# Performance work log

Measured on AMD Instinct MI355X. Metric: run time of the kernel, lower is better.

## Reference

```python
import jax, jax.numpy as jnp
import numpy as np

N = 100000
E = 1600000
D_IN = 128
D_OUT = 128
HEADS = 4
C = D_OUT // HEADS  # per-head channels = 32
NEG_SLOPE = 0.2
EPS_SOFTMAX = 1e-16
EPS_LN = 1e-5


def setup_inputs() -> dict:
    key = jax.random.key(0)
    ks = jax.random.split(key, 10)
    x = jax.random.normal(ks[0], (N, D_IN), dtype=jnp.float32)
    edge_index = jax.random.randint(ks[1], (2, E), 0, N, dtype=jnp.int64)
    s = 1.0 / np.sqrt(D_IN)
    W = jax.random.normal(ks[2], (D_IN, HEADS * C), dtype=jnp.float32) * s
    att_src = jax.random.normal(ks[3], (HEADS, C), dtype=jnp.float32) * (1.0 / np.sqrt(C))
    att_dst = jax.random.normal(ks[4], (HEADS, C), dtype=jnp.float32) * (1.0 / np.sqrt(C))
    gat_bias = jax.random.normal(ks[5], (D_OUT,), dtype=jnp.float32) * 0.02
    skip_W = jax.random.normal(ks[6], (D_IN, D_OUT), dtype=jnp.float32) * s
    skip_b = jax.random.normal(ks[7], (D_OUT,), dtype=jnp.float32) * 0.02
    ln_g = jnp.ones((D_OUT,), dtype=jnp.float32)
    ln_b = jnp.zeros((D_OUT,), dtype=jnp.float32)
    return {"x": x, "edge_index": edge_index, "W": W, "att_src": att_src,
            "att_dst": att_dst, "gat_bias": gat_bias, "skip_W": skip_W,
            "skip_b": skip_b, "ln_g": ln_g, "ln_b": ln_b}


def _gat_edge_conv(x, src, dst, W, att_src, att_dst, gat_bias, skip_W, skip_b, ln_g, ln_b):
    n = x.shape[0]
    h = (x @ W).reshape(n, HEADS, C)                      # [N,H,C]
    a_s = jnp.einsum('nhc,hc->nh', h, att_src)            # [N,H]
    a_d = jnp.einsum('nhc,hc->nh', h, att_dst)            # [N,H]
    e = jax.nn.leaky_relu(a_s[src] + a_d[dst], NEG_SLOPE)  # [E,H]
    # segment softmax over incoming edges of each dst node
    m = jax.ops.segment_max(e, dst, num_segments=n)        # [N,H]
    p = jnp.exp(e - m[dst])
    z = jax.ops.segment_sum(p, dst, num_segments=n)        # [N,H]
    alpha = p / (z[dst] + EPS_SOFTMAX)                     # [E,H]
    msg = h[src] * alpha[:, :, None]                       # [E,H,C]
    out = jax.ops.segment_sum(msg, dst, num_segments=n)    # [N,H,C]
    out = out.reshape(n, HEADS * C) + gat_bias
    out = out + x @ skip_W + skip_b
    mu = out.mean(-1, keepdims=True)
    var = ((out - mu) ** 2).mean(-1, keepdims=True)
    return (out - mu) * jax.lax.rsqrt(var + EPS_LN) * ln_g + ln_b


def reference(x, edge_index, W, att_src, att_dst, gat_bias, skip_W, skip_b, ln_g, ln_b):
    n = x.shape[0]
    loops = jnp.arange(n, dtype=edge_index.dtype)          # PyG GATConv add_self_loops=True
    src = jnp.concatenate([edge_index[0], loops])
    dst = jnp.concatenate([edge_index[1], loops])
    return _gat_edge_conv(x, src, dst, W, att_src, att_dst, gat_bias, skip_W, skip_b, ln_g, ln_b)
```

## Files before the change

### kernel.cpp

```cpp
#include <hip/hip_runtime.h>
#include <hip/hip_bf16.h>

#define D 128
#define HEADS 4
#define NEG_SLOPE 0.2f
#define QSCALE 0.0625f
#define QUNSCALE 16.0f

#define BCAP64 1280
#define NB_HIST 1600
#define BCHUNK 4096
#define LDSPAD 136

typedef __attribute__((ext_vector_type(8))) short short8;
typedef __attribute__((ext_vector_type(4))) float f32x4;
typedef __attribute__((ext_vector_type(2))) float f32x2;
typedef __attribute__((ext_vector_type(2))) _Float16 h2;

__device__ __forceinline__ float lrelu(float v) {
    return fmaxf(v, NEG_SLOPE * v);
}

__device__ __forceinline__ short f2bf(float v) {
    __hip_bfloat16 b = __float2bfloat16(v);
    short s;
    __builtin_memcpy(&s, &b, 2);
    return s;
}

__device__ __forceinline__ unsigned short f2h(float v) {
    _Float16 h = (_Float16)v;
    unsigned short s;
    __builtin_memcpy(&s, &h, 2);
    return s;
}

__global__ __launch_bounds__(256)
void wprep_kernel(const float* __restrict__ W, const float* __restrict__ S,
                  short* __restrict__ wsT, int* __restrict__ woffA, int nb64) {
    const int idx = blockIdx.x * 256 + threadIdx.x;
    const int nn = idx >> 7, k = idx & 127;
    const float v = (nn < 128) ? W[k * D + nn] : S[k * D + (nn - 128)];
    wsT[idx] = f2bf(v);
    if (idx < nb64) woffA[idx] = 0;
}

__global__ __launch_bounds__(512, 4)
void big_kernel(const float* __restrict__ x, const short* __restrict__ wsT,
                const float* __restrict__ skip_b, const float* __restrict__ gat_bias,
                const float* __restrict__ att_src, const float* __restrict__ att_dst,
                unsigned short* __restrict__ hb, unsigned short* __restrict__ baseb,
                float* __restrict__ a_s, float* __restrict__ a_d,
                const int* __restrict__ ei, int* __restrict__ woffA,
                unsigned int* __restrict__ pairs,
                int n, int E_, int nb64, int BA) {
    __shared__ __align__(16) char smem[64 * LDSPAD * 2];
    const int t = threadIdx.x;
    if ((int)blockIdx.x < BA) {
        int* hist = (int*)smem;
        int* gbase = hist + NB_HIST;
        for (int q = t; q < nb64; q += 512) hist[q] = 0;
        __syncthreads();
        int sv[8], dv[8], rk[8];
        const int base = blockIdx.x * BCHUNK;
        #pragma unroll
        for (int i = 0; i < 8; ++i) {
            const int e = base + i * 512 + t;
            if (e < E_) {
                sv[i] = ei[e];
                dv[i] = ei[E_ + e];
                rk[i] = atomicAdd(&hist[dv[i] >> 6], 1);
            } else {
                sv[i] = -1;
            }
        }
        __syncthreads();
        for (int q = t; q < nb64; q += 512) {
            const int v = hist[q];
            gbase[q] = v ? (q * BCAP64 + atomicAdd(&woffA[q], v)) : 0;
        }
        __syncthreads();
        #pragma unroll
        for (int i = 0; i < 8; ++i) {
            if (sv[i] >= 0) {
                const int q = dv[i] >> 6;
                const unsigned int pos = (unsigned int)(gbase[q] + rk[i]);
                if (pos < (unsigned int)(q + 1) * BCAP64)
                    pairs[pos] = ((unsigned int)sv[i] << 6) | (unsigned int)(dv[i] & 63);
            }
        }
        return;
    }
    short (*xs)[LDSPAD] = (short(*)[LDSPAD])smem;
    const int row0 = (blockIdx.x - BA) * 64;
    #pragma unroll
    for (int i = 0; i < 4; ++i) {
        const int f = t + 512 * i;
        const int row = f >> 5, c4 = (f & 31) * 4;
        float4 v = make_float4(0.f, 0.f, 0.f, 0.f);
        if (row0 + row < n) v = *(const float4*)&x[(size_t)(row0 + row) * D + c4];
        short4 s4;
        s4.x = f2bf(v.x); s4.y = f2bf(v.y); s4.z = f2bf(v.z); s4.w = f2bf(v.w);
        *(short4*)&xs[row][c4] = s4;
    }
    __syncthreads();
    const int wv = t >> 6, lane = t & 63;
    const int lo = lane & 15, hi = lane >> 4;
    const int wr = wv >> 2;
    const int wc = wv & 3;
    f32x4 acc[2][4] = {};
    #pragma unroll
    for (int k0 = 0; k0 < 128; k0 += 32) {
        const int kk = k0 + hi * 8;
        short8 a0 = *(const short8*)&xs[wr * 32 + lo][kk];
        short8 a1 = *(const short8*)&xs[wr * 32 + 16 + lo][kk];
        #pragma unroll
        for (int nt = 0; nt < 4; ++nt) {
            short8 b = *(const short8*)&wsT[(wc * 64 + nt * 16 + lo) * D + kk];
            acc[0][nt] = __builtin_amdgcn_mfma_f32_16x16x32_bf16(b, a0, acc[0][nt], 0, 0, 0);
            acc[1][nt] = __builtin_amdgcn_mfma_f32_16x16x32_bf16(b, a1, acc[1][nt], 0, 0, 0);
        }
    }
    if (wc < 2) {
        float4 av[4], dv4[4];
        #pragma unroll
        for (int nt = 0; nt < 4; ++nt) {
            const int c0 = wc * 64 + nt * 16 + hi * 4;
            av[nt] = *(const float4*)&att_src[c0];
            dv4[nt] = *(const float4*)&att_dst[c0];
        }
        #pragma unroll
        for (int mt = 0; mt < 2; ++mt) {
            float ps0 = acc[mt][0][0] * av[0].x + acc[mt][0][1] * av[0].y
                      + acc[mt][0][2] * av[0].z + acc[mt][0][3] * av[0].w
                      + acc[mt][1][0] * av[1].x + acc[mt][1][1] * av[1].y
                      + acc[mt][1][2] * av[1].z + acc[mt][1][3] * av[1].w;
            float ps1 = acc[mt][2][0] * av[2].x + acc[mt][2][1] * av[2].y
                      + acc[mt][2][2] * av[2].z + acc[mt][2][3] * av[2].w
                      + acc[mt][3][0] * av[3].x + acc[mt][3][1] * av[3].y
                      + acc[mt][3][2] * av[3].z + acc[mt][3][3] * av[3].w;
            float pd0 = acc[mt][0][0] * dv4[0].x + acc[mt][0][1] * dv4[0].y
                      + acc[mt][0][2] * dv4[0].z + acc[mt][0][3] * dv4[0].w
                      + acc[mt][1][0] * dv4[1].x + acc[mt][1][1] * dv4[1].y
                      + acc[mt][1][2] * dv4[1].z + acc[mt][1][3] * dv4[1].w;
            float pd1 = acc[mt][2][0] * dv4[2].x + acc[mt][2][1] * dv4[2].y
                      + acc[mt][2][2] * dv4[2].z + acc[mt][2][3] * dv4[2].w
                      + acc[mt][3][0] * dv4[3].x + acc[mt][3][1] * dv4[3].y
                      + acc[mt][3][2] * dv4[3].z + acc[mt][3][3] * dv4[3].w;
            ps0 += __shfl_xor(ps0, 16, 64); ps0 += __shfl_xor(ps0, 32, 64);
            ps1 += __shfl_xor(ps1, 16, 64); ps1 += __shfl_xor(ps1, 32, 64);
            pd0 += __shfl_xor(pd0, 16, 64); pd0 += __shfl_xor(pd0, 32, 64);
            pd1 += __shfl_xor(pd1, 16, 64); pd1 += __shfl_xor(pd1, 32, 64);
            if (lane < 16) {
                const int r = row0 + wr * 32 + mt * 16 + lane;
                if (r < n) {
                    a_s[r * HEADS + wc * 2 + 0] = ps0;
                    a_s[r * HEADS + wc * 2 + 1] = ps1;
                    a_d[r * HEADS + wc * 2 + 0] = pd0;
                    a_d[r * HEADS + wc * 2 + 1] = pd1;
                }
            }
        }
    }
    #pragma unroll
    for (int mt = 0; mt < 2; ++mt) {
        const int r = row0 + wr * 32 + mt * 16 + lo;
        if (r >= n) continue;
        #pragma unroll
        for (int nt = 0; nt < 4; ++nt) {
            const int cc0 = wc * 64 + nt * 16 + hi * 4;
            const bool isH = cc0 < 128;
            const int c0 = isH ? cc0 : cc0 - 128;
            float4 bb = make_float4(0.f, 0.f, 0.f, 0.f);
            if (!isH) {
                const float4 sb = *(const float4*)&skip_b[c0];
                const float4 gb = *(const float4*)&gat_bias[c0];
                bb.x = sb.x + gb.x; bb.y = sb.y + gb.y;
                bb.z = sb.z + gb.z; bb.w = sb.w + gb.w;
            }
            unsigned short* dst = isH ? hb : baseb;
            short4 s4;
            s4.x = f2h(acc[mt][nt][0] + bb.x);
            s4.y = f2h(acc[mt][nt][1] + bb.y);
            s4.z = f2h(acc[mt][nt][2] + bb.z);
            s4.w = f2h(acc[mt][nt][3] + bb.w);
            *(short4*)&dst[(size_t)r * D + c0] = s4;
        }
    }
}

__global__ __launch_bounds__(512)
void binB_kernel(const unsigned int* __restrict__ pairs, const int* __restrict__ wcur,
                 int* __restrict__ cnt, int* __restrict__ offs,
                 int* __restrict__ ssrc, int n, int nb64) {
    __shared__ int lds[320];
    const int t = threadIdx.x;
    const int sub = t >> 8, tt = t & 255;
    int* nh = lds + sub * 160;
    int* sc = lds + sub * 160 + 80;
    const int qb = blockIdx.x * 2 + sub;
    const bool valid = qb < nb64;
    const int sbeg = valid ? qb * BCAP64 : 0;
    int total = valid ? wcur[qb] : 0;
    if (total > BCAP64) total = BCAP64;
    const int send = sbeg + total;
    if (tt < 64) nh[tt] = 0;
    __syncthreads();
    unsigned int pk[6];
    int rk[6];
    int nl = 0;
    #pragma unroll
    for (int r = 0; r < 5; ++r) {
        const int e = sbeg + r * 256 + tt;
        if (e < send) {
            const unsigned int p = pairs[e];
            const int rr = atomicAdd(&nh[p & 63], 1);
            pk[nl] = p; rk[nl] = rr; ++nl;
        }
    }
    __syncthreads();
    const int v = (tt < 64) ? nh[tt] : 0;
    if (tt < 64) sc[tt] = v;
    __syncthreads();
    for (int off = 1; off < 64; off <<= 1) {
        const int xv = (tt >= off && tt < 64) ? sc[tt - off] : 0;
        __syncthreads();
        if (tt < 64) sc[tt] += xv;
        __syncthreads();
    }
    const int ex = (tt < 64) ? sc[tt] - v : 0;
    if (tt < 64 && valid) {
        const int node = qb * 64 + tt;
        if (node < n) { cnt[node] = v; offs[node] = sbeg + ex; }
    }
    __syncthreads();
    if (tt < 64) nh[tt] = ex;
    __syncthreads();
    for (int i = 0; i < nl; ++i)
        ssrc[sbeg + nh[pk[i] & 63] + rk[i]] = (int)(pk[i] >> 6);
}

__global__ __launch_bounds__(256)
void gather_kernel(const int* __restrict__ offs, const int* __restrict__ cnt,
                   const int* __restrict__ ssrc, const float* __restrict__ a_s,
                   const float* __restrict__ a_d, const uint4* __restrict__ hb16,
                   const uint4* __restrict__ baseb16,
                   const float* __restrict__ ln_g, const float* __restrict__ ln_b,
                   float* __restrict__ out, int n) {
    const int lane = threadIdx.x & 63;
    const int i = blockIdx.x * 4 + (threadIdx.x >> 6);
    if (i >= n) return;
    const int e4 = lane >> 2, h4 = lane & 3;
    const int l15 = lane & 15;
    const int grp = lane >> 4;
    const int hh = l15 >> 2;
    const uint4 bv = baseb16[(size_t)i * 16 + l15];
    const float2 g2 = ((const float2*)ln_g)[l15 * 4 + grp];
    const float2 lb2 = ((const float2*)ln_b)[l15 * 4 + grp];
    const float as_h4 = a_s[i * HEADS + h4];
    const float ad_h4 = a_d[i * HEADS + h4];
    const float qself = __expf(lrelu(as_h4 + ad_h4));
    float zacc = (e4 == 0) ? qself : 0.f;
    h2 acc0 = {0.f, 0.f}, acc1 = {0.f, 0.f}, acc2 = {0.f, 0.f}, acc3 = {0.f, 0.f};
    {
        const float qs = __shfl(qself, hh, 64) * QSCALE;
        if (grp == 0) {
            const uint4 u = hb16[(size_t)i * 16 + l15];
            const _Float16 wh = (_Float16)qs;
            const h2 w2 = {wh, wh};
            acc0 = __builtin_bit_cast(h2, u.x) * w2;
            acc1 = __builtin_bit_cast(h2, u.y) * w2;
            acc2 = __builtin_bit_cast(h2, u.z) * w2;
            acc3 = __builtin_bit_cast(h2, u.w) * w2;
        }
    }
    const int o = offs[i];
    const int c = cnt[i];
    for (int k0 = 0; k0 < c; k0 += 16) {
        const int rem = c - k0;
        int srow = 0;
        float q = 0.f;
        if (e4 < rem) {
            const int sidx = ssrc[o + k0 + e4];
            srow = sidx << 4;
            q = __expf(lrelu(a_s[sidx * HEADS + h4] + ad_h4));
        }
        zacc += q;
        const _Float16 qh = (_Float16)(q * QSCALE);
        const h2 qv = {qh, qh};
        const int qpk = __builtin_bit_cast(int, qv);
        const int m = rem < 16 ? rem : 16;
        int ee = 0;
// ... 36 lines not shown
        acc2 += __builtin_bit_cast(h2, __shfl_xor(__builtin_bit_cast(int, acc2), off, 64));
        acc3 += __builtin_bit_cast(h2, __shfl_xor(__builtin_bit_cast(int, acc3), off, 64));
    }
    #pragma unroll
    for (int off = 4; off < 64; off <<= 1) zacc += __shfl_xor(zacc, off, 64);
    const float zz = __shfl(zacc, hh, 64);
    const float rz = QUNSCALE / (zz + 1e-16f);
    const h2 b0 = __builtin_bit_cast(h2, bv.x);
    const h2 b1 = __builtin_bit_cast(h2, bv.y);
    const h2 b2 = __builtin_bit_cast(h2, bv.z);
    const h2 b3 = __builtin_bit_cast(h2, bv.w);
    const float v0 = (float)acc0.x * rz + (float)b0.x;
    const float v1 = (float)acc0.y * rz + (float)b0.y;
    const float v2 = (float)acc1.x * rz + (float)b1.x;
    const float v3 = (float)acc1.y * rz + (float)b1.y;
    const float v4 = (float)acc2.x * rz + (float)b2.x;
    const float v5 = (float)acc2.y * rz + (float)b2.y;
    const float v6 = (float)acc3.x * rz + (float)b3.x;
    const float v7 = (float)acc3.y * rz + (float)b3.y;
    float s1 = v0 + v1 + v2 + v3 + v4 + v5 + v6 + v7;
    float s2 = v0 * v0 + v1 * v1 + v2 * v2 + v3 * v3
             + v4 * v4 + v5 * v5 + v6 * v6 + v7 * v7;
    #pragma unroll
    for (int off = 1; off < 16; off <<= 1) {
        s1 += __shfl_xor(s1, off, 64);
        s2 += __shfl_xor(s2, off, 64);
    }
    const float mu = s1 * (1.f / 128.f);
    const float var = s2 * (1.f / 128.f) - mu * mu;
    const float r = rsqrtf(var + 1e-5f);
    const float lo = grp == 0 ? v0 : grp == 1 ? v2 : grp == 2 ? v4 : v6;
    const float hi = grp == 0 ? v1 : grp == 1 ? v3 : grp == 2 ? v5 : v7;
    f32x2 o2;
    o2.x = (lo - mu) * r * g2.x + lb2.x;
    o2.y = (hi - mu) * r * g2.y + lb2.y;
    __builtin_nontemporal_store(o2, (f32x2*)out + ((size_t)i * 64 + l15 * 4 + grp));
}

extern "C" void kernel_launch(void* const* d_in, const int* in_sizes, int n_in,
                              void* d_out, int out_size, void* d_ws, size_t ws_size,
                              hipStream_t stream) {
    const float* x        = (const float*)d_in[0];
    const int*   ei       = (const int*)d_in[1];
    const float* W        = (const float*)d_in[2];
    const float* att_src  = (const float*)d_in[3];
    const float* att_dst  = (const float*)d_in[4];
    const float* gat_bias = (const float*)d_in[5];
    const float* skip_W   = (const float*)d_in[6];
    const float* skip_b   = (const float*)d_in[7];
    const float* ln_g     = (const float*)d_in[8];
    const float* ln_b     = (const float*)d_in[9];
    float* out = (float*)d_out;

    const int n    = in_sizes[0] / D;
    const int E_   = in_sizes[1] / 2;
    const int nb64 = (n + 63) >> 6;
    const int nbbB = (nb64 + 1) >> 1;

    char* p = (char*)d_ws;
    auto carve = [&p](size_t bytes) {
        char* r = p;
        p += (bytes + 255) & ~(size_t)255;
        return r;
    };
    short* wsT            = (short*)carve(32768 * sizeof(short));
    unsigned short* hb    = (unsigned short*)carve((size_t)n * D * 2);
    unsigned short* baseb = (unsigned short*)carve((size_t)n * D * 2);
    float* a_s            = (float*)carve((size_t)n * HEADS * 4);
    float* a_d            = (float*)carve((size_t)n * HEADS * 4);
    int*   cnt            = (int*)carve((size_t)n * 4);
    int*   offs           = (int*)carve((size_t)n * 4);
    int*   woffA          = (int*)carve((size_t)nb64 * 4);
    int*   ssrc           = (int*)carve((size_t)nb64 * BCAP64 * 4);
    unsigned int* pairs   = (unsigned int*)carve((size_t)nb64 * BCAP64 * 4);

    wprep_kernel<<<128, 256, 0, stream>>>(W, skip_W, wsT, woffA, nb64);
    const int BA = (E_ + BCHUNK - 1) / BCHUNK;
    const int ngemm = (n + 63) / 64;
    big_kernel<<<BA + ngemm, 512, 0, stream>>>(x, wsT, skip_b, gat_bias,
                                               att_src, att_dst,
                                               hb, baseb, a_s, a_d,
                                               ei, woffA, pairs,
                                               n, E_, nb64, BA);
    binB_kernel<<<nbbB, 512, 0, stream>>>(pairs, woffA, cnt, offs, ssrc, n, nb64);
    gather_kernel<<<(n + 3) / 4, 256, 0, stream>>>(offs, cnt, ssrc, a_s, a_d,
                                                   (const uint4*)hb,
                                                   (const uint4*)baseb,
                                                   ln_g, ln_b, out, n);
}
```

Before: 273.0 us.

## Fuse weight prep, binning, GEMM into persistent kernel with grid barrier

Replaces the wprep, big_kernel and binB launches with one persistent 768-block kernel. Phase one does the edge histogram binning and the weight transpose. A global atomic spin barrier follows, then phase two runs the per-bucket sort and a 32-row GEMM tile. The aim is to remove launch gaps and the tail between kernels, and to overlap the GEMM with the bucket sort. It adds a memset, a software grid barrier that relies on all 768 blocks being co-resident (deadlock risk otherwise), and smaller GEMM tiles that reload the weights more often.

```diff
diff --git a/kernel.cpp b/kernel.cpp
--- a/kernel.cpp
+++ b/kernel.cpp
@@ -11,6 +11,7 @@
 #define NB_HIST 1600
 #define BCHUNK 4096
 #define LDSPAD 136
+#define NBLK 768
 
 typedef __attribute__((ext_vector_type(8))) short short8;
 typedef __attribute__((ext_vector_type(4))) float f32x4;
@@ -35,209 +36,218 @@
     return s;
 }
 
-__global__ __launch_bounds__(256)
-void wprep_kernel(const float* __restrict__ W, const float* __restrict__ S,
-                  short* __restrict__ wsT, int* __restrict__ woffA, int nb64) {
-    const int idx = blockIdx.x * 256 + threadIdx.x;
-    const int nn = idx >> 7, k = idx & 127;
-    const float v = (nn < 128) ? W[k * D + nn] : S[k * D + (nn - 128)];
-    wsT[idx] = f2bf(v);
-    if (idx < nb64) woffA[idx] = 0;
-}
-
-__global__ __launch_bounds__(512, 4)
-void big_kernel(const float* __restrict__ x, const short* __restrict__ wsT,
-                const float* __restrict__ skip_b, const float* __restrict__ gat_bias,
-                const float* __restrict__ att_src, const float* __restrict__ att_dst,
-                unsigned short* __restrict__ hb, unsigned short* __restrict__ baseb,
-                float* __restrict__ a_s, float* __restrict__ a_d,
-                const int* __restrict__ ei, int* __restrict__ woffA,
-                unsigned int* __restrict__ pairs,
-                int n, int E_, int nb64, int BA) {
-    __shared__ __align__(16) char smem[64 * LDSPAD * 2];
+__global__ __launch_bounds__(256, 4)
+void fused_mid(const float* __restrict__ x, const float* __restrict__ W,
+               const float* __restrict__ S, short* __restrict__ wsT,
+               const float* __restrict__ skip_b, const float* __restrict__ gat_bias,
+               const float* __restrict__ att_src, const float* __restrict__ att_dst,
+               unsigned short* __restrict__ hb, unsigned short* __restrict__ baseb,
+               float* __restrict__ a_s, float* __restrict__ a_d,
+               const int* __restrict__ ei, int* __restrict__ woffA,
+               unsigned int* __restrict__ pairs,
+               int* __restrict__ cnt, int* __restrict__ offs, int* __restrict__ ssrc,
+               int* __restrict__ bar,
+               int n, int E_, int nb64, int BA, int ngemm) {
+    __shared__ __align__(16) char smem[12800];
     const int t = threadIdx.x;
-    if ((int)blockIdx.x < BA) {
-        int* hist = (int*)smem;
-        int* gbase = hist + NB_HIST;
-        for (int q = t; q < nb64; q += 512) hist[q] = 0;
+    const int bid = blockIdx.x;
+
+    const int ATOT = BA + 128;
+    for (int vb = bid; vb < ATOT; vb += NBLK) {
+        if (vb < BA) {
+            int* hist = (int*)smem;
+            int* gbase = hist + NB_HIST;
+            for (int q = t; q < nb64; q += 256) hist[q] = 0;
+            __syncthreads();
+            int sv[16], dv[16], rk[16];
+            const int base = vb * BCHUNK;
+            #pragma unroll
+            for (int i = 0; i < 16; ++i) {
+                const int e = base + i * 256 + t;
+                if (e < E_) {
+                    sv[i] = ei[e];
+                    dv[i] = ei[E_ + e];
+                    rk[i] = atomicAdd(&hist[dv[i] >> 6], 1);
+                } else {
+                    sv[i] = -1;
+                }
+            }
+            __syncthreads();
+            for (int q = t; q < nb64; q += 256) {
+                const int v = hist[q];
+                gbase[q] = v ? (q * BCAP64 + atomicAdd(&woffA[q], v)) : 0;
+            }
+            __syncthreads();
+            #pragma unroll
+            for (int i = 0; i < 16; ++i) {
+                if (sv[i] >= 0) {
+                    const int q = dv[i] >> 6;
+                    const unsigned int pos = (unsigned int)(gbase[q] + rk[i]);
+                    if (pos < (unsigned int)(q + 1) * BCAP64)
+                        pairs[pos] = ((unsigned int)sv[i] << 6) | (unsigned int)(dv[i] & 63);
+                }
+            }
+            __syncthreads();
+        } else {
+            const int idx = (vb - BA) * 256 + t;
+            const int nn = idx >> 7, k = idx & 127;
+            const float v = (nn < 128) ? W[k * D + nn] : S[k * D + (nn - 128)];
+            wsT[idx] = f2bf(v);
+        }
+    }
+
+    __syncthreads();
+    if (t == 0) {
+        __threadfence();
+        atomicAdd(bar, 1);
+        while (__hip_atomic_load(bar, __ATOMIC_RELAXED, __HIP_MEMORY_SCOPE_AGENT) < NBLK)
+            __builtin_amdgcn_s_sleep(8);
+    }
+    __syncthreads();
+    __threadfence();
+
+    const int BTOT = nb64 + ngemm;
+    for (int vb = bid; vb < BTOT; vb += NBLK) {
+        if (vb < nb64) {
+            int* nh = (int*)smem;
+            int* sc = nh + 80;
+            const int qb = vb;
+            const int sbeg = qb * BCAP64;
+            int total = woffA[qb];
+            if (total > BCAP64) total = BCAP64;
+            const int send = sbeg + total;
+            if (t < 64) nh[t] = 0;
+            __syncthreads();
+            unsigned int pk[5];
+            int rk[5];
+            int nl = 0;
+            #pragma unroll
+            for (int r = 0; r < 5; ++r) {
+                const int e = sbeg + r * 256 + t;
+                if (e < send) {
+                    const unsigned int p = pairs[e];
+                    const int rr = atomicAdd(&nh[p & 63], 1);
+                    pk[nl] = p; rk[nl] = rr; ++nl;
+                }
+            }
+            __syncthreads();
+            const int v = (t < 64) ? nh[t] : 0;
+            if (t < 64) sc[t] = v;
+            __syncthreads();
+            for (int off = 1; off < 64; off <<= 1) {
+                const int xv = (t >= off && t < 64) ? sc[t - off] : 0;
+                __syncthreads();
+                if (t < 64) sc[t] += xv;
+                __syncthreads();
+            }
+            const int ex = (t < 64) ? sc[t] - v : 0;
+            if (t < 64) {
+                const int node = qb * 64 + t;
+                if (node < n) { cnt[node] = v; offs[node] = sbeg + ex; }
+            }
+            __syncthreads();
+            if (t < 64) nh[t] = ex;
+            __syncthreads();
+            for (int i = 0; i < nl; ++i)
+                ssrc[sbeg + nh[pk[i] & 63] + rk[i]] = (int)(pk[i] >> 6);
+        } else {
+            short (*xs)[LDSPAD] = (short(*)[LDSPAD])smem;
+            const int row0 = (vb - nb64) * 32;
+            #pragma unroll
+            for (int i = 0; i < 4; ++i) {
+                const int f = t + 256 * i;
+                const int row = f >> 5, c4 = (f & 31) * 4;
+                float4 v = make_float4(0.f, 0.f, 0.f, 0.f);
+                if (row0 + row < n) v = *(const float4*)&x[(size_t)(row0 + row) * D + c4];
+                short4 s4;
+                s4.x = f2bf(v.x); s4.y = f2bf(v.y); s4.z = f2bf(v.z); s4.w = f2bf(v.w);
+                *(short4*)&xs[row][c4] = s4;
+            }
+            __syncthreads();
+            const int wc = t >> 6, lane = t & 63;
+            const int lo = lane & 15, hi = lane >> 4;
+            f32x4 acc[2][4] = {};
+            #pragma unroll
+            for (int k0 = 0; k0 < 128; k0 += 32) {
+                const int kk = k0 + hi * 8;
+                short8 a0 = *(const short8*)&xs[lo][kk];
+                short8 a1 = *(const short8*)&xs[16 + lo][kk];
+                #pragma unroll
+                for (int nt = 0; nt < 4; ++nt) {
+                    short8 b = *(const short8*)&wsT[(wc * 64 + nt * 16 + lo) * D + kk];
+                    acc[0][nt] = __builtin_amdgcn_mfma_f32_16x16x32_bf16(b, a0, acc[0][nt], 0, 0, 0);
+                    acc[1][nt] = __builtin_amdgcn_mfma_f32_16x16x32_bf16(b, a1, acc[1][nt], 0, 0, 0);
+                }
+            }
+            if (wc < 2) {
+                float4 av[4], dv4[4];
+                #pragma unroll
+                for (int nt = 0; nt < 4; ++nt) {
+                    const int c0 = wc * 64 + nt * 16 + hi * 4;
+                    av[nt] = *(const float4*)&att_src[c0];
+                    dv4[nt] = *(const float4*)&att_dst[c0];
+                }
+                #pragma unroll
+                for (int mt = 0; mt < 2; ++mt) {
+                    float ps0 = acc[mt][0][0] * av[0].x + acc[mt][0][1] * av[0].y
+                              + acc[mt][0][2] * av[0].z + acc[mt][0][3] * av[0].w
+                              + acc[mt][1][0] * av[1].x + acc[mt][1][1] * av[1].y
+                              + acc[mt][1][2] * av[1].z + acc[mt][1][3] * av[1].w;
+                    float ps1 = acc[mt][2][0] * av[2].x + acc[mt][2][1] * av[2].y
+                              + acc[mt][2][2] * av[2].z + acc[mt][2][3] * av[2].w
+                              + acc[mt][3][0] * av[3].x + acc[mt][3][1] * av[3].y
+                              + acc[mt][3][2] * av[3].z + acc[mt][3][3] * av[3].w;
+                    float pd0 = acc[mt][0][0] * dv4[0].x + acc[mt][0][1] * dv4[0].y
+                              + acc[mt][0][2] * dv4[0].z + acc[mt][0][3] * dv4[0].w
+                              + acc[mt][1][0] * dv4[1].x + acc[mt][1][1] * dv4[1].y
+                              + acc[mt][1][2] * dv4[1].z + acc[mt][1][3] * dv4[1].w;
+                    float pd1 = acc[mt][2][0] * dv4[2].x + acc[mt][2][1] * dv4[2].y
+                              + acc[mt][2][2] * dv4[2].z + acc[mt][2][3] * dv4[2].w
+                              + acc[mt][3][0] * dv4[3].x + acc[mt][3][1] * dv4[3].y
+                              + acc[mt][3][2] * dv4[3].z + acc[mt][3][3] * dv4[3].w;
+                    ps0 += __shfl_xor(ps0, 16, 64); ps0 += __shfl_xor(ps0, 32, 64);
+                    ps1 += __shfl_xor(ps1, 16, 64); ps1 += __shfl_xor(ps1, 32, 64);
+                    pd0 += __shfl_xor(pd0, 16, 64); pd0 += __shfl_xor(pd0, 32, 64);
+                    pd1 += __shfl_xor(pd1, 16, 64); pd1 += __shfl_xor(pd1, 32, 64);
+                    if (lane < 16) {
+                        const int r = row0 + mt * 16 + lane;
+                        if (r < n) {
+                            a_s[r * HEADS + wc * 2 + 0] = ps0;
+                            a_s[r * HEADS + wc * 2 + 1] = ps1;
+                            a_d[r * HEADS + wc * 2 + 0] = pd0;
+                            a_d[r * HEADS + wc * 2 + 1] = pd1;
+                        }
+                    }
+                }
+            }
+            #pragma unroll
+            for (int mt = 0; mt < 2; ++mt) {
+                const int r = row0 + mt * 16 + lo;
+                if (r >= n) continue;
+                #pragma unroll
+                for (int nt = 0; nt < 4; ++nt) {
+                    const int cc0 = wc * 64 + nt * 16 + hi * 4;
+                    const bool isH = cc0 < 128;
+                    const int c0 = isH ? cc0 : cc0 - 128;
+                    float4 bb = make_float4(0.f, 0.f, 0.f, 0.f);
+                    if (!isH) {
+                        const float4 sb = *(const float4*)&skip_b[c0];
+                        const float4 gb = *(const float4*)&gat_bias[c0];
+                        bb.x = sb.x + gb.x; bb.y = sb.y + gb.y;
+                        bb.z = sb.z + gb.z; bb.w = sb.w + gb.w;
+                    }
+                    unsigned short* dst = isH ? hb : baseb;
+                    short4 s4;
+                    s4.x = f2h(acc[mt][nt][0] + bb.x);
+                    s4.y = f2h(acc[mt][nt][1] + bb.y);
+                    s4.z = f2h(acc[mt][nt][2] + bb.z);
+                    s4.w = f2h(acc[mt][nt][3] + bb.w);
+                    *(short4*)&dst[(size_t)r * D + c0] = s4;
+                }
+            }
+        }
         __syncthreads();
-        int sv[8], dv[8], rk[8];
-        const int base = blockIdx.x * BCHUNK;
-        #pragma unroll
-        for (int i = 0; i < 8; ++i) {
-            const int e = base + i * 512 + t;
-            if (e < E_) {
-                sv[i] = ei[e];
-                dv[i] = ei[E_ + e];
-                rk[i] = atomicAdd(&hist[dv[i] >> 6], 1);
-            } else {
-                sv[i] = -1;
-            }
-        }
-        __syncthreads();
-        for (int q = t; q < nb64; q += 512) {
-            const int v = hist[q];
-            gbase[q] = v ? (q * BCAP64 + atomicAdd(&woffA[q], v)) : 0;
-        }
-        __syncthreads();
-        #pragma unroll
-        for (int i = 0; i < 8; ++i) {
-            if (sv[i] >= 0) {
-                const int q = dv[i] >> 6;
-                const unsigned int pos = (unsigned int)(gbase[q] + rk[i]);
-                if (pos < (unsigned int)(q + 1) * BCAP64)
-                    pairs[pos] = ((unsigned int)sv[i] << 6) | (unsigned int)(dv[i] & 63);
-            }
-        }
-        return;
-    }
-    short (*xs)[LDSPAD] = (short(*)[LDSPAD])smem;
-    const int row0 = (blockIdx.x - BA) * 64;
-    #pragma unroll
-    for (int i = 0; i < 4; ++i) {
-        const int f = t + 512 * i;
-        const int row = f >> 5, c4 = (f & 31) * 4;
-        float4 v = make_float4(0.f, 0.f, 0.f, 0.f);
-        if (row0 + row < n) v = *(const float4*)&x[(size_t)(row0 + row) * D + c4];
-        short4 s4;
-        s4.x = f2bf(v.x); s4.y = f2bf(v.y); s4.z = f2bf(v.z); s4.w = f2bf(v.w);
-        *(short4*)&xs[row][c4] = s4;
-    }
-    __syncthreads();
-    const int wv = t >> 6, lane = t & 63;
-    const int lo = lane & 15, hi = lane >> 4;
-    const int wr = wv >> 2;
-    const int wc = wv & 3;
-    f32x4 acc[2][4] = {};
-    #pragma unroll
-    for (int k0 = 0; k0 < 128; k0 += 32) {
-        const int kk = k0 + hi * 8;
-        short8 a0 = *(const short8*)&xs[wr * 32 + lo][kk];
-        short8 a1 = *(const short8*)&xs[wr * 32 + 16 + lo][kk];
-        #pragma unroll
-        for (int nt = 0; nt < 4; ++nt) {
-            short8 b = *(const short8*)&wsT[(wc * 64 + nt * 16 + lo) * D + kk];
-            acc[0][nt] = __builtin_amdgcn_mfma_f32_16x16x32_bf16(b, a0, acc[0][nt], 0, 0, 0);
-            acc[1][nt] = __builtin_amdgcn_mfma_f32_16x16x32_bf16(b, a1, acc[1][nt], 0, 0, 0);
-        }
-    }
-    if (wc < 2) {
-        float4 av[4], dv4[4];
-        #pragma unroll
-        for (int nt = 0; nt < 4; ++nt) {
-            const int c0 = wc * 64 + nt * 16 + hi * 4;
-            av[nt] = *(const float4*)&att_src[c0];
-            dv4[nt] = *(const float4*)&att_dst[c0];
-        }
-        #pragma unroll
-        for (int mt = 0; mt < 2; ++mt) {
-            float ps0 = acc[mt][0][0] * av[0].x + acc[mt][0][1] * av[0].y
-                      + acc[mt][0][2] * av[0].z + acc[mt][0][3] * av[0].w
-                      + acc[mt][1][0] * av[1].x + acc[mt][1][1] * av[1].y
-                      + acc[mt][1][2] * av[1].z + acc[mt][1][3] * av[1].w;
-            float ps1 = acc[mt][2][0] * av[2].x + acc[mt][2][1] * av[2].y
-                      + acc[mt][2][2] * av[2].z + acc[mt][2][3] * av[2].w
-                      + acc[mt][3][0] * av[3].x + acc[mt][3][1] * av[3].y
-                      + acc[mt][3][2] * av[3].z + acc[mt][3][3] * av[3].w;
-            float pd0 = acc[mt][0][0] * dv4[0].x + acc[mt][0][1] * dv4[0].y
-                      + acc[mt][0][2] * dv4[0].z + acc[mt][0][3] * dv4[0].w
-                      + acc[mt][1][0] * dv4[1].x + acc[mt][1][1] * dv4[1].y
-                      + acc[mt][1][2] * dv4[1].z + acc[mt][1][3] * dv4[1].w;
-            float pd1 = acc[mt][2][0] * dv4[2].x + acc[mt][2][1] * dv4[2].y
-                      + acc[mt][2][2] * dv4[2].z + acc[mt][2][3] * dv4[2].w
-                      + acc[mt][3][0] * dv4[3].x + acc[mt][3][1] * dv4[3].y
-                      + acc[mt][3][2] * dv4[3].z + acc[mt][3][3] * dv4[3].w;
-            ps0 += __shfl_xor(ps0, 16, 64); ps0 += __shfl_xor(ps0, 32, 64);
-            ps1 += __shfl_xor(ps1, 16, 64); ps1 += __shfl_xor(ps1, 32, 64);
-            pd0 += __shfl_xor(pd0, 16, 64); pd0 += __shfl_xor(pd0, 32, 64);
-            pd1 += __shfl_xor(pd1, 16, 64); pd1 += __shfl_xor(pd1, 32, 64);
-            if (lane < 16) {
-                const int r = row0 + wr * 32 + mt * 16 + lane;
-                if (r < n) {
-                    a_s[r * HEADS + wc * 2 + 0] = ps0;
-                    a_s[r * HEADS + wc * 2 + 1] = ps1;
-                    a_d[r * HEADS + wc * 2 + 0] = pd0;
-                    a_d[r * HEADS + wc * 2 + 1] = pd1;
-                }
-            }
-        }
-    }
-    #pragma unroll
-    for (int mt = 0; mt < 2; ++mt) {
-        const int r = row0 + wr * 32 + mt * 16 + lo;
-        if (r >= n) continue;
-        #pragma unroll
-        for (int nt = 0; nt < 4; ++nt) {
-            const int cc0 = wc * 64 + nt * 16 + hi * 4;
-            const bool isH = cc0 < 128;
-            const int c0 = isH ? cc0 : cc0 - 128;
-            float4 bb = make_float4(0.f, 0.f, 0.f, 0.f);
-            if (!isH) {
-                const float4 sb = *(const float4*)&skip_b[c0];
-                const float4 gb = *(const float4*)&gat_bias[c0];
-                bb.x = sb.x + gb.x; bb.y = sb.y + gb.y;
-                bb.z = sb.z + gb.z; bb.w = sb.w + gb.w;
-            }
-            unsigned short* dst = isH ? hb : baseb;
-            short4 s4;
-            s4.x = f2h(acc[mt][nt][0] + bb.x);
-            s4.y = f2h(acc[mt][nt][1] + bb.y);
-            s4.z = f2h(acc[mt][nt][2] + bb.z);
-            s4.w = f2h(acc[mt][nt][3] + bb.w);
-            *(short4*)&dst[(size_t)r * D + c0] = s4;
-        }
-    }
-}
-
-__global__ __launch_bounds__(512)
-void binB_kernel(const unsigned int* __restrict__ pairs, const int* __restrict__ wcur,
-                 int* __restrict__ cnt, int* __restrict__ offs,
-                 int* __restrict__ ssrc, int n, int nb64) {
-    __shared__ int lds[320];
-    const int t = threadIdx.x;
-    const int sub = t >> 8, tt = t & 255;
-    int* nh = lds + sub * 160;
-    int* sc = lds + sub * 160 + 80;
-    const int qb = blockIdx.x * 2 + sub;
-    const bool valid = qb < nb64;
-    const int sbeg = valid ? qb * BCAP64 : 0;
-    int total = valid ? wcur[qb] : 0;
-    if (total > BCAP64) total = BCAP64;
-    const int send = sbeg + total;
-    if (tt < 64) nh[tt] = 0;
-    __syncthreads();
-    unsigned int pk[6];
-    int rk[6];
-    int nl = 0;
-    #pragma unroll
-    for (int r = 0; r < 5; ++r) {
-        const int e = sbeg + r * 256 + tt;
-        if (e < send) {
-            const unsigned int p = pairs[e];
-            const int rr = atomicAdd(&nh[p & 63], 1);
-            pk[nl] = p; rk[nl] = rr; ++nl;
-        }
-    }
-    __syncthreads();
-    const int v = (tt < 64) ? nh[tt] : 0;
-    if (tt < 64) sc[tt] = v;
-    __syncthreads();
-    for (int off = 1; off < 64; off <<= 1) {
-        const int xv = (tt >= off && tt < 64) ? sc[tt - off] : 0;
-        __syncthreads();
-        if (tt < 64) sc[tt] += xv;
-        __syncthreads();
-    }
-    const int ex = (tt < 64) ? sc[tt] - v : 0;
-    if (tt < 64 && valid) {
-        const int node = qb * 64 + tt;
-        if (node < n) { cnt[node] = v; offs[node] = sbeg + ex; }
-    }
-    __syncthreads();
-    if (tt < 64) nh[tt] = ex;
-    __syncthreads();
-    for (int i = 0; i < nl; ++i)
-        ssrc[sbeg + nh[pk[i] & 63] + rk[i]] = (int)(pk[i] >> 6);
+    }
 }
 
 __global__ __launch_bounds__(256)
@@ -383,7 +393,6 @@
     const int n    = in_sizes[0] / D;
     const int E_   = in_sizes[1] / 2;
     const int nb64 = (n + 63) >> 6;
-    const int nbbB = (nb64 + 1) >> 1;
 
     char* p = (char*)d_ws;
     auto carve = [&p](size_t bytes) {
@@ -398,19 +407,19 @@
     float* a_d            = (float*)carve((size_t)n * HEADS * 4);
     int*   cnt            = (int*)carve((size_t)n * 4);
     int*   offs           = (int*)carve((size_t)n * 4);
-    int*   woffA          = (int*)carve((size_t)nb64 * 4);
+    int*   woffA          = (int*)carve(((size_t)nb64 + 8) * 4);
+    int*   bar            = woffA + nb64;
     int*   ssrc           = (int*)carve((size_t)nb64 * BCAP64 * 4);
     unsigned int* pairs   = (unsigned int*)carve((size_t)nb64 * BCAP64 * 4);
 
-    wprep_kernel<<<128, 256, 0, stream>>>(W, skip_W, wsT, woffA, nb64);
+    hipMemsetAsync(woffA, 0, ((size_t)nb64 + 8) * 4, stream);
+
     const int BA = (E_ + BCHUNK - 1) / BCHUNK;
-    const int ngemm = (n + 63) / 64;
-    big_kernel<<<BA + ngemm, 512, 0, stream>>>(x, wsT, skip_b, gat_bias,
-                                               att_src, att_dst,
-                                               hb, baseb, a_s, a_d,
-                                               ei, woffA, pairs,
-                                               n, E_, nb64, BA);
-    binB_kernel<<<nbbB, 512, 0, stream>>>(pairs, woffA, cnt, offs, ssrc, n, nb64);
+    const int ngemm = (n + 31) / 32;
+    fused_mid<<<NBLK, 256, 0, stream>>>(x, W, skip_W, wsT, skip_b, gat_bias,
+                                        att_src, att_dst, hb, baseb, a_s, a_d,
+                                        ei, woffA, pairs, cnt, offs, ssrc, bar,
+                                        n, E_, nb64, BA, ngemm);
     gather_kernel<<<(n + 3) / 4, 256, 0, stream>>>(offs, cnt, ssrc, a_s, a_d,
                                                    (const uint4*)hb,
                                                    (const uint4*)baseb,
```

After: 423.3 us. +55.1%, slower.

## Replace bucketed edge binning with global-atomic CSR build and staged GEMM stores

Applied to the files above, without the earlier changes.

Replaces the two-level bucketed edge binning (per-block LDS histograms into fixed-capacity 64-node buckets, then a per-bucket sort) with a plain CSR build. The GEMM kernel counts in-degrees with global atomics, a scan kernel computes offsets and claims block bases through a global atomic cursor, and a scatter kernel places sources with per-node atomics. GEMM outputs are now staged through LDS so rows are written with coalesced 16-byte stores. This drops the bucket capacity limit and the pairs buffer, but adds a kernel launch, contended global atomics, and leaves neighbor order within each node nondeterministic.

```diff
diff --git a/kernel.cpp b/kernel.cpp
--- a/kernel.cpp
+++ b/kernel.cpp
@@ -6,11 +6,8 @@
 #define NEG_SLOPE 0.2f
 #define QSCALE 0.0625f
 #define QUNSCALE 16.0f
-
-#define BCAP64 1280
-#define NB_HIST 1600
-#define BCHUNK 4096
 #define LDSPAD 136
+#define OUTPAD 264
 
 typedef __attribute__((ext_vector_type(8))) short short8;
 typedef __attribute__((ext_vector_type(4))) float f32x4;
@@ -37,62 +34,28 @@
 
 __global__ __launch_bounds__(256)
 void wprep_kernel(const float* __restrict__ W, const float* __restrict__ S,
-                  short* __restrict__ wsT, int* __restrict__ woffA, int nb64) {
+                  short* __restrict__ wsT, int* __restrict__ cnt,
+                  int* __restrict__ gcur, int n) {
     const int idx = blockIdx.x * 256 + threadIdx.x;
     const int nn = idx >> 7, k = idx & 127;
     const float v = (nn < 128) ? W[k * D + nn] : S[k * D + (nn - 128)];
     wsT[idx] = f2bf(v);
-    if (idx < nb64) woffA[idx] = 0;
+    for (int j = idx; j < n; j += 32768) cnt[j] = 0;
+    if (idx == 0) *gcur = 0;
 }
 
 __global__ __launch_bounds__(512, 4)
-void big_kernel(const float* __restrict__ x, const short* __restrict__ wsT,
-                const float* __restrict__ skip_b, const float* __restrict__ gat_bias,
-                const float* __restrict__ att_src, const float* __restrict__ att_dst,
-                unsigned short* __restrict__ hb, unsigned short* __restrict__ baseb,
-                float* __restrict__ a_s, float* __restrict__ a_d,
-                const int* __restrict__ ei, int* __restrict__ woffA,
-                unsigned int* __restrict__ pairs,
-                int n, int E_, int nb64, int BA) {
-    __shared__ __align__(16) char smem[64 * LDSPAD * 2];
+void gemmhist_kernel(const float* __restrict__ x, const short* __restrict__ wsT,
+                     const float* __restrict__ skip_b, const float* __restrict__ gat_bias,
+                     const float* __restrict__ att_src, const float* __restrict__ att_dst,
+                     unsigned short* __restrict__ hb, unsigned short* __restrict__ baseb,
+                     float* __restrict__ a_s, float* __restrict__ a_d,
+                     const int* __restrict__ ei, int* __restrict__ cnt,
+                     int n, int E_) {
+    __shared__ __align__(16) short smem[64 * OUTPAD];
+    short (*xs)[LDSPAD] = (short(*)[LDSPAD])smem;
     const int t = threadIdx.x;
-    if ((int)blockIdx.x < BA) {
-        int* hist = (int*)smem;
-        int* gbase = hist + NB_HIST;
-        for (int q = t; q < nb64; q += 512) hist[q] = 0;
-        __syncthreads();
-        int sv[8], dv[8], rk[8];
-        const int base = blockIdx.x * BCHUNK;
-        #pragma unroll
-        for (int i = 0; i < 8; ++i) {
-            const int e = base + i * 512 + t;
-            if (e < E_) {
-                sv[i] = ei[e];
-                dv[i] = ei[E_ + e];
-                rk[i] = atomicAdd(&hist[dv[i] >> 6], 1);
-            } else {
-                sv[i] = -1;
-            }
-        }
-        __syncthreads();
-        for (int q = t; q < nb64; q += 512) {
-            const int v = hist[q];
-            gbase[q] = v ? (q * BCAP64 + atomicAdd(&woffA[q], v)) : 0;
-        }
-        __syncthreads();
-        #pragma unroll
-        for (int i = 0; i < 8; ++i) {
-            if (sv[i] >= 0) {
-                const int q = dv[i] >> 6;
-                const unsigned int pos = (unsigned int)(gbase[q] + rk[i]);
-                if (pos < (unsigned int)(q + 1) * BCAP64)
-                    pairs[pos] = ((unsigned int)sv[i] << 6) | (unsigned int)(dv[i] & 63);
-            }
-        }
-        return;
-    }
-    short (*xs)[LDSPAD] = (short(*)[LDSPAD])smem;
-    const int row0 = (blockIdx.x - BA) * 64;
+    const int row0 = blockIdx.x * 64;
     #pragma unroll
     for (int i = 0; i < 4; ++i) {
         const int f = t + 512 * i;
@@ -162,82 +125,82 @@
             }
         }
     }
+    __syncthreads();
+    short (*ot)[OUTPAD] = (short(*)[OUTPAD])smem;
     #pragma unroll
     for (int mt = 0; mt < 2; ++mt) {
-        const int r = row0 + wr * 32 + mt * 16 + lo;
-        if (r >= n) continue;
+        const int row = wr * 32 + mt * 16 + lo;
         #pragma unroll
         for (int nt = 0; nt < 4; ++nt) {
             const int cc0 = wc * 64 + nt * 16 + hi * 4;
-            const bool isH = cc0 < 128;
-            const int c0 = isH ? cc0 : cc0 - 128;
             float4 bb = make_float4(0.f, 0.f, 0.f, 0.f);
-            if (!isH) {
-                const float4 sb = *(const float4*)&skip_b[c0];
-                const float4 gb = *(const float4*)&gat_bias[c0];
+            if (cc0 >= 128) {
+                const float4 sb = *(const float4*)&skip_b[cc0 - 128];
+                const float4 gb = *(const float4*)&gat_bias[cc0 - 128];
                 bb.x = sb.x + gb.x; bb.y = sb.y + gb.y;
                 bb.z = sb.z + gb.z; bb.w = sb.w + gb.w;
             }
-            unsigned short* dst = isH ? hb : baseb;
             short4 s4;
             s4.x = f2h(acc[mt][nt][0] + bb.x);
             s4.y = f2h(acc[mt][nt][1] + bb.y);
             s4.z = f2h(acc[mt][nt][2] + bb.z);
             s4.w = f2h(acc[mt][nt][3] + bb.w);
-            *(short4*)&dst[(size_t)r * D + c0] = s4;
-        }
-    }
+            *(short4*)&ot[row][cc0] = s4;
+        }
+    }
+    __syncthreads();
+    #pragma unroll
+    for (int j = 0; j < 4; ++j) {
+        const int c = j * 512 + t;
+        const int row = c >> 5, ch = c & 31;
+        const int r = row0 + row;
+        if (r < n) {
+            const uint4 v = *(const uint4*)&ot[row][ch * 8];
+            unsigned short* dst = (ch < 16) ? hb : baseb;
+            *(uint4*)&dst[(size_t)r * D + (ch & 15) * 8] = v;
+        }
+    }
+    const int gid = blockIdx.x * 512 + t;
+    const int gsz = gridDim.x * 512;
+    for (int e = gid; e < E_; e += gsz) atomicAdd(&cnt[ei[E_ + e]], 1);
 }
 
 __global__ __launch_bounds__(512)
-void binB_kernel(const unsigned int* __restrict__ pairs, const int* __restrict__ wcur,
-                 int* __restrict__ cnt, int* __restrict__ offs,
-                 int* __restrict__ ssrc, int n, int nb64) {
-    __shared__ int lds[320];
+void scan_kernel(const int* __restrict__ cnt, int* __restrict__ offs,
+                 int* __restrict__ cur, int* __restrict__ gcur, int n) {
+    __shared__ int sc[512];
+    __shared__ int base_s;
     const int t = threadIdx.x;
-    const int sub = t >> 8, tt = t & 255;
-    int* nh = lds + sub * 160;
-    int* sc = lds + sub * 160 + 80;
-    const int qb = blockIdx.x * 2 + sub;
-    const bool valid = qb < nb64;
-    const int sbeg = valid ? qb * BCAP64 : 0;
-    int total = valid ? wcur[qb] : 0;
-    if (total > BCAP64) total = BCAP64;
-    const int send = sbeg + total;
-    if (tt < 64) nh[tt] = 0;
-    __syncthreads();
-    unsigned int pk[6];
-    int rk[6];
-    int nl = 0;
-    #pragma unroll
-    for (int r = 0; r < 5; ++r) {
-        const int e = sbeg + r * 256 + tt;
-        if (e < send) {
-            const unsigned int p = pairs[e];
-            const int rr = atomicAdd(&nh[p & 63], 1);
-            pk[nl] = p; rk[nl] = rr; ++nl;
-        }
-    }
-    __syncthreads();
-    const int v = (tt < 64) ? nh[tt] : 0;
-    if (tt < 64) sc[tt] = v;
-    __syncthreads();
-    for (int off = 1; off < 64; off <<= 1) {
-        const int xv = (tt >= off && tt < 64) ? sc[tt - off] : 0;
+    const int node = blockIdx.x * 512 + t;
+    const int v = (node < n) ? cnt[node] : 0;
+    sc[t] = v;
+    __syncthreads();
+    for (int off = 1; off < 512; off <<= 1) {
+        const int xv = (t >= off) ? sc[t - off] : 0;
         __syncthreads();
-        if (tt < 64) sc[tt] += xv;
+        sc[t] += xv;
         __syncthreads();
     }
-    const int ex = (tt < 64) ? sc[tt] - v : 0;
-    if (tt < 64 && valid) {
-        const int node = qb * 64 + tt;
-        if (node < n) { cnt[node] = v; offs[node] = sbeg + ex; }
-    }
-    __syncthreads();
-    if (tt < 64) nh[tt] = ex;
-    __syncthreads();
-    for (int i = 0; i < nl; ++i)
-        ssrc[sbeg + nh[pk[i] & 63] + rk[i]] = (int)(pk[i] >> 6);
+    if (t == 511) base_s = atomicAdd(gcur, sc[511]);
+    __syncthreads();
+    if (node < n) {
+        const int ex = base_s + sc[t] - v;
+        offs[node] = ex;
+        cur[node] = ex;
+    }
+}
+
+__global__ __launch_bounds__(256)
+void scatter_kernel(const int* __restrict__ ei, int* __restrict__ cur,
+                    int* __restrict__ ssrc, int E_) {
+    const int gid = blockIdx.x * 256 + threadIdx.x;
+    const int gsz = gridDim.x * 256;
+    for (int e = gid; e < E_; e += gsz) {
+        const int sv = ei[e];
+        const int dvv = ei[E_ + e];
+        const int pos = atomicAdd(&cur[dvv], 1);
+        ssrc[pos] = sv;
+    }
 }
 
 __global__ __launch_bounds__(256)
@@ -380,10 +343,8 @@
     const float* ln_b     = (const float*)d_in[9];
     float* out = (float*)d_out;
 
-    const int n    = in_sizes[0] / D;
-    const int E_   = in_sizes[1] / 2;
-    const int nb64 = (n + 63) >> 6;
-    const int nbbB = (nb64 + 1) >> 1;
+    const int n  = in_sizes[0] / D;
+    const int E_ = in_sizes[1] / 2;
 
     char* p = (char*)d_ws;
     auto carve = [&p](size_t bytes) {
@@ -398,19 +359,18 @@
     float* a_d            = (float*)carve((size_t)n * HEADS * 4);
     int*   cnt            = (int*)carve((size_t)n * 4);
     int*   offs           = (int*)carve((size_t)n * 4);
-    int*   woffA          = (int*)carve((size_t)nb64 * 4);
-    int*   ssrc           = (int*)carve((size_t)nb64 * BCAP64 * 4);
-    unsigned int* pairs   = (unsigned int*)carve((size_t)nb64 * BCAP64 * 4);
-
-    wprep_kernel<<<128, 256, 0, stream>>>(W, skip_W, wsT, woffA, nb64);
-    const int BA = (E_ + BCHUNK - 1) / BCHUNK;
+    int*   cur            = (int*)carve((size_t)n * 4);
+    int*   gcur           = (int*)carve(256);
+    int*   ssrc           = (int*)carve((size_t)E_ * 4);
+
+    wprep_kernel<<<128, 256, 0, stream>>>(W, skip_W, wsT, cnt, gcur, n);
     const int ngemm = (n + 63) / 64;
-    big_kernel<<<BA + ngemm, 512, 0, stream>>>(x, wsT, skip_b, gat_bias,
+    gemmhist_kernel<<<ngemm, 512, 0, stream>>>(x, wsT, skip_b, gat_bias,
                                                att_src, att_dst,
                                                hb, baseb, a_s, a_d,
-                                               ei, woffA, pairs,
-                                               n, E_, nb64, BA);
-    binB_kernel<<<nbbB, 512, 0, stream>>>(pairs, woffA, cnt, offs, ssrc, n, nb64);
+                                               ei, cnt, n, E_);
+    scan_kernel<<<(n + 511) / 512, 512, 0, stream>>>(cnt, offs, cur, gcur, n);
+    scatter_kernel<<<1024, 256, 0, stream>>>(ei, cur, ssrc, E_);
     gather_kernel<<<(n + 3) / 4, 256, 0, stream>>>(offs, cnt, ssrc, a_s, a_d,
                                                    (const uint4*)hb,
                                                    (const uint4*)baseb,
```

Measured after the change: 403.8 us. 47.9% more time.

## Move coarse edge binning to prep kernel and fuse fine binning with GEMM

Applied to the files above, without the earlier changes.

Coarse edge binning (histogram plus scatter into pairs) moves out of the GEMM kernel and into a prep kernel that also converts the weights. The fine per-node binning now shares a launch with the GEMM blocks instead of running as its own kernel, so the total kernel count stays the same. The prep kernel handles 16 edges per thread with 256-thread blocks, and the woffA zeroing becomes a memset. The goal is to overlap the second binning pass with the GEMM, at the cost of an extra memset launch and more register pressure in prep.

```diff
diff --git a/kernel.cpp b/kernel.cpp
--- a/kernel.cpp
+++ b/kernel.cpp
@@ -9,7 +9,9 @@
 
 #define BCAP64 1280
 #define NB_HIST 1600
-#define BCHUNK 4096
+#define BEPT 16
+#define BCHUNK (256 * BEPT)
+#define WPREP_BLOCKS 128
 #define LDSPAD 136
 
 typedef __attribute__((ext_vector_type(8))) short short8;
@@ -36,63 +38,117 @@
 }
 
 __global__ __launch_bounds__(256)
-void wprep_kernel(const float* __restrict__ W, const float* __restrict__ S,
-                  short* __restrict__ wsT, int* __restrict__ woffA, int nb64) {
-    const int idx = blockIdx.x * 256 + threadIdx.x;
-    const int nn = idx >> 7, k = idx & 127;
-    const float v = (nn < 128) ? W[k * D + nn] : S[k * D + (nn - 128)];
-    wsT[idx] = f2bf(v);
-    if (idx < nb64) woffA[idx] = 0;
+void prep_kernel(const float* __restrict__ W, const float* __restrict__ S,
+                 short* __restrict__ wsT,
+                 const int* __restrict__ ei, int* __restrict__ woffA,
+                 unsigned int* __restrict__ pairs, int E_, int nb64, int BA) {
+    const int t = threadIdx.x;
+    if ((int)blockIdx.x >= BA) {
+        const int idx = (blockIdx.x - BA) * 256 + t;
+        const int nn = idx >> 7, k = idx & 127;
+        const float v = (nn < 128) ? W[k * D + nn] : S[k * D + (nn - 128)];
+        wsT[idx] = f2bf(v);
+        return;
+    }
+    __shared__ int hist[NB_HIST];
+    __shared__ int gbase[NB_HIST];
+    for (int q = t; q < nb64; q += 256) hist[q] = 0;
+    __syncthreads();
+    int sv[BEPT], dv[BEPT], rk[BEPT];
+    const int base = blockIdx.x * BCHUNK;
+    #pragma unroll
+    for (int i = 0; i < BEPT; ++i) {
+        const int e = base + i * 256 + t;
+        if (e < E_) {
+            sv[i] = ei[e];
+            dv[i] = ei[E_ + e];
+            rk[i] = atomicAdd(&hist[dv[i] >> 6], 1);
+        } else {
+            sv[i] = -1;
+        }
+    }
+    __syncthreads();
+    for (int q = t; q < nb64; q += 256) {
+        const int v = hist[q];
+        gbase[q] = v ? (q * BCAP64 + atomicAdd(&woffA[q], v)) : 0;
+    }
+    __syncthreads();
+    #pragma unroll
+    for (int i = 0; i < BEPT; ++i) {
+        if (sv[i] >= 0) {
+            const int q = dv[i] >> 6;
+            const unsigned int pos = (unsigned int)(gbase[q] + rk[i]);
+            if (pos < (unsigned int)(q + 1) * BCAP64)
+                pairs[pos] = ((unsigned int)sv[i] << 6) | (unsigned int)(dv[i] & 63);
+        }
+    }
 }
 
 __global__ __launch_bounds__(512, 4)
-void big_kernel(const float* __restrict__ x, const short* __restrict__ wsT,
+void mid_kernel(const float* __restrict__ x, const short* __restrict__ wsT,
                 const float* __restrict__ skip_b, const float* __restrict__ gat_bias,
                 const float* __restrict__ att_src, const float* __restrict__ att_dst,
                 unsigned short* __restrict__ hb, unsigned short* __restrict__ baseb,
                 float* __restrict__ a_s, float* __restrict__ a_d,
-                const int* __restrict__ ei, int* __restrict__ woffA,
-                unsigned int* __restrict__ pairs,
-                int n, int E_, int nb64, int BA) {
+                const unsigned int* __restrict__ pairs, const int* __restrict__ wcur,
+                int* __restrict__ cnt, int* __restrict__ offs, int* __restrict__ ssrc,
+                int n, int nb64, int nbbB) {
     __shared__ __align__(16) char smem[64 * LDSPAD * 2];
     const int t = threadIdx.x;
-    if ((int)blockIdx.x < BA) {
-        int* hist = (int*)smem;
-        int* gbase = hist + NB_HIST;
-        for (int q = t; q < nb64; q += 512) hist[q] = 0;
+    if ((int)blockIdx.x < nbbB) {
+        int* lds = (int*)smem;
+        const int sub = t >> 8, tt = t & 255;
+        int* nh = lds + sub * 160;
+        int* sc = lds + sub * 160 + 80;
+        const int qb = blockIdx.x * 2 + sub;
+        const bool valid = qb < nb64;
+        const int sbeg = valid ? qb * BCAP64 : 0;
+        int total = valid ? wcur[qb] : 0;
+        if (total > BCAP64) total = BCAP64;
+        const int send = sbeg + total;
+        if (tt < 64) nh[tt] = 0;
         __syncthreads();
-        int sv[8], dv[8], rk[8];
-        const int base = blockIdx.x * BCHUNK;
-        #pragma unroll
-        for (int i = 0; i < 8; ++i) {
-            const int e = base + i * 512 + t;
-            if (e < E_) {
-                sv[i] = ei[e];
-                dv[i] = ei[E_ + e];
-                rk[i] = atomicAdd(&hist[dv[i] >> 6], 1);
-            } else {
-                sv[i] = -1;
-            }
-        }
+        const int e0 = sbeg + tt;
+        const int e1 = e0 + 256, e2 = e1 + 256, e3 = e2 + 256, e4 = e3 + 256;
+        unsigned int p0 = 0, p1 = 0, p2 = 0, p3 = 0, p4 = 0;
+        if (e0 < send) p0 = pairs[e0];
+        if (e1 < send) p1 = pairs[e1];
+        if (e2 < send) p2 = pairs[e2];
+        if (e3 < send) p3 = pairs[e3];
+        if (e4 < send) p4 = pairs[e4];
+        int r0 = -1, r1 = -1, r2 = -1, r3 = -1, r4 = -1;
+        if (e0 < send) r0 = atomicAdd(&nh[p0 & 63], 1);
+        if (e1 < send) r1 = atomicAdd(&nh[p1 & 63], 1);
+        if (e2 < send) r2 = atomicAdd(&nh[p2 & 63], 1);
+        if (e3 < send) r3 = atomicAdd(&nh[p3 & 63], 1);
+        if (e4 < send) r4 = atomicAdd(&nh[p4 & 63], 1);
         __syncthreads();
-        for (int q = t; q < nb64; q += 512) {
-            const int v = hist[q];
-            gbase[q] = v ? (q * BCAP64 + atomicAdd(&woffA[q], v)) : 0;
-        }
+        const int v = (tt < 64) ? nh[tt] : 0;
+        if (tt < 64) sc[tt] = v;
         __syncthreads();
-        #pragma unroll
-        for (int i = 0; i < 8; ++i) {
-            if (sv[i] >= 0) {
-                const int q = dv[i] >> 6;
-                const unsigned int pos = (unsigned int)(gbase[q] + rk[i]);
-                if (pos < (unsigned int)(q + 1) * BCAP64)
-                    pairs[pos] = ((unsigned int)sv[i] << 6) | (unsigned int)(dv[i] & 63);
-            }
-        }
+        for (int off = 1; off < 64; off <<= 1) {
+            const int xv = (tt >= off && tt < 64) ? sc[tt - off] : 0;
+            __syncthreads();
+            if (tt < 64) sc[tt] += xv;
+            __syncthreads();
+        }
+        const int ex = (tt < 64) ? sc[tt] - v : 0;
+        if (tt < 64 && valid) {
+            const int node = qb * 64 + tt;
+            if (node < n) { cnt[node] = v; offs[node] = sbeg + ex; }
+        }
+        __syncthreads();
+        if (tt < 64) nh[tt] = ex;
+        __syncthreads();
+        if (r0 >= 0) ssrc[sbeg + nh[p0 & 63] + r0] = (int)(p0 >> 6);
+        if (r1 >= 0) ssrc[sbeg + nh[p1 & 63] + r1] = (int)(p1 >> 6);
+        if (r2 >= 0) ssrc[sbeg + nh[p2 & 63] + r2] = (int)(p2 >> 6);
+        if (r3 >= 0) ssrc[sbeg + nh[p3 & 63] + r3] = (int)(p3 >> 6);
+        if (r4 >= 0) ssrc[sbeg + nh[p4 & 63] + r4] = (int)(p4 >> 6);
         return;
     }
     short (*xs)[LDSPAD] = (short(*)[LDSPAD])smem;
-    const int row0 = (blockIdx.x - BA) * 64;
+    const int row0 = (blockIdx.x - nbbB) * 64;
     #pragma unroll
     for (int i = 0; i < 4; ++i) {
         const int f = t + 512 * i;
@@ -187,57 +243,6 @@
             *(short4*)&dst[(size_t)r * D + c0] = s4;
         }
     }
-}
-
-__global__ __launch_bounds__(512)
-void binB_kernel(const unsigned int* __restrict__ pairs, const int* __restrict__ wcur,
-                 int* __restrict__ cnt, int* __restrict__ offs,
-                 int* __restrict__ ssrc, int n, int nb64) {
-    __shared__ int lds[320];
-    const int t = threadIdx.x;
-    const int sub = t >> 8, tt = t & 255;
-    int* nh = lds + sub * 160;
-    int* sc = lds + sub * 160 + 80;
-    const int qb = blockIdx.x * 2 + sub;
-    const bool valid = qb < nb64;
-    const int sbeg = valid ? qb * BCAP64 : 0;
-    int total = valid ? wcur[qb] : 0;
-    if (total > BCAP64) total = BCAP64;
-    const int send = sbeg + total;
-    if (tt < 64) nh[tt] = 0;
-    __syncthreads();
-    unsigned int pk[6];
-    int rk[6];
-    int nl = 0;
-    #pragma unroll
-    for (int r = 0; r < 5; ++r) {
-        const int e = sbeg + r * 256 + tt;
-        if (e < send) {
-            const unsigned int p = pairs[e];
-            const int rr = atomicAdd(&nh[p & 63], 1);
-            pk[nl] = p; rk[nl] = rr; ++nl;
-        }
-    }
-    __syncthreads();
-    const int v = (tt < 64) ? nh[tt] : 0;
-    if (tt < 64) sc[tt] = v;
-    __syncthreads();
-    for (int off = 1; off < 64; off <<= 1) {
-        const int xv = (tt >= off && tt < 64) ? sc[tt - off] : 0;
-        __syncthreads();
-        if (tt < 64) sc[tt] += xv;
-        __syncthreads();
-    }
-    const int ex = (tt < 64) ? sc[tt] - v : 0;
-    if (tt < 64 && valid) {
-        const int node = qb * 64 + tt;
-        if (node < n) { cnt[node] = v; offs[node] = sbeg + ex; }
-    }
-    __syncthreads();
-    if (tt < 64) nh[tt] = ex;
-    __syncthreads();
-    for (int i = 0; i < nl; ++i)
-        ssrc[sbeg + nh[pk[i] & 63] + rk[i]] = (int)(pk[i] >> 6);
 }
 
 __global__ __launch_bounds__(256)
@@ -402,15 +407,17 @@
     int*   ssrc           = (int*)carve((size_t)nb64 * BCAP64 * 4);
     unsigned int* pairs   = (unsigned int*)carve((size_t)nb64 * BCAP64 * 4);
 
-    wprep_kernel<<<128, 256, 0, stream>>>(W, skip_W, wsT, woffA, nb64);
+    hipMemsetAsync(woffA, 0, (size_t)nb64 * 4, stream);
+
     const int BA = (E_ + BCHUNK - 1) / BCHUNK;
+    prep_kernel<<<BA + WPREP_BLOCKS, 256, 0, stream>>>(W, skip_W, wsT, ei, woffA,
+                                                       pairs, E_, nb64, BA);
     const int ngemm = (n + 63) / 64;
-    big_kernel<<<BA + ngemm, 512, 0, stream>>>(x, wsT, skip_b, gat_bias,
-                                               att_src, att_dst,
-                                               hb, baseb, a_s, a_d,
-                                               ei, woffA, pairs,
-                                               n, E_, nb64, BA);
-    binB_kernel<<<nbbB, 512, 0, stream>>>(pairs, woffA, cnt, offs, ssrc, n, nb64);
+    mid_kernel<<<nbbB + ngemm, 512, 0, stream>>>(x, wsT, skip_b, gat_bias,
+                                                 att_src, att_dst,
+                                                 hb, baseb, a_s, a_d,
+                                                 pairs, woffA,
+                                                 cnt, offs, ssrc, n, nb64, nbbB);
     gather_kernel<<<(n + 3) / 4, 256, 0, stream>>>(offs, cnt, ssrc, a_s, a_d,
                                                    (const uint4*)hb,
                                                    (const uint4*)baseb,
```

After: 277.7 us. About the same (+1.7%).
